# Performance work log

Measured on AMD Instinct MI355X. Metric: run time of the kernel, lower is better.

Reference implementation:

```python
import jax, jax.numpy as jnp
import numpy as np

B, KL, XL, DIM, H, PB = 4, 128, 4096, 256, 8, 8
HD = DIM // H
SCALE = HD ** -0.5
N_DIS = 64 + 2


def setup_inputs() -> dict:
    key = jax.random.key(0)
    ks = jax.random.split(key, 10)
    x = jax.random.normal(ks[0], (B, XL, DIM), jnp.float32)
    kernal = jax.random.normal(ks[1], (B, KL, DIM), jnp.float32)
    rd = jax.random.randint(ks[2], (B, KL, XL), 0, N_DIS)
    polar_pos = jax.random.randint(ks[3], (B, KL, XL), 0, PB)
    att_mask = jax.random.uniform(ks[4], (B, H, XL, KL)) < 0.1
    W_qkv = jax.random.normal(ks[5], (DIM, 3 * DIM), jnp.float32) * 0.02
    dis_embed = jax.random.normal(ks[6], (N_DIS, H), jnp.float32) * 0.02
    polar_emb = jax.random.normal(ks[7], (PB, 1), jnp.float32) * 0.02
    W_proj = jax.random.normal(ks[8], (DIM, DIM), jnp.float32) * 0.02
    b_proj = jnp.zeros((DIM,), jnp.float32)
    return dict(x=x, kernal=kernal, rd=rd, polar_pos=polar_pos, att_mask=att_mask,
                W_qkv=W_qkv, dis_embed=dis_embed, polar_emb=polar_emb,
                W_proj=W_proj, b_proj=b_proj)


def _heads(t, h):
    b, n, d = t.shape
    return t.reshape(b, n, h, d // h).transpose(0, 2, 1, 3)  # b h n hd


def reference(x, kernal, rd, polar_pos, att_mask, W_qkv, dis_embed, polar_emb, W_proj, b_proj):
    b, xl, dim = x.shape
    kl = kernal.shape[1]
    h = H
    scale = (dim // h) ** -0.5

    q, k, v = [_heads(t, h) for t in jnp.split(x @ W_qkv, 3, axis=-1)]        # b h xl hd
    k_q, k_k, k_v = [_heads(t, h) for t in jnp.split(kernal @ W_qkv, 3, axis=-1)]  # b h kl hd

    rd_e = dis_embed[rd].transpose(0, 3, 1, 2)  # (b,kl,xl,h) -> (b,h,kl,xl)

    # kernel -> x attention scores
    k_x_attn = jnp.einsum('bhkd,bhxd->bhkx', k_q, k) * scale  # b h kl xl

    # main orientation: one-hot-weighted |attn| reduced over x, argmax over polar bins
    pp = jnp.broadcast_to(polar_pos[:, None], (b, h, kl, xl))  # b h kl xl
    polar_hot = jax.nn.one_hot(pp, PB, dtype=k_x_attn.dtype)   # b h kl xl o
    ori_sum = jnp.einsum('bhkx,bhkxo->bhko', jnp.abs(k_x_attn), polar_hot)
    main_ori = jnp.argmax(ori_sum, axis=-1)                    # b h kl
    new_polar = pp - main_ori[..., None]
    new_polar = jnp.where(new_polar < 0, new_polar + PB, new_polar)
    polar_bias = polar_emb[new_polar, 0]                       # b h kl xl

    mask_k = att_mask.transpose(0, 1, 3, 2)                    # b h kl xl
    k_x_attn = jnp.where(mask_k, jnp.asarray(-1e6, k_x_attn.dtype), k_x_attn)
    attn_k = jax.nn.softmax(k_x_attn + rd_e + polar_bias, axis=-1)
    k_out = jnp.einsum('bhkx,bhxd->bhkd', attn_k, v)
    k_out = k_out.transpose(0, 2, 1, 3).reshape(b, kl, dim) @ W_proj + b_proj

    # x -> kernel attention scores
    x_k_attn = jnp.einsum('bhxd,bhkd->bhxk', q, k_k) * scale   # b h xl kl
    x_k_attn = jnp.where(att_mask, jnp.asarray(-1e9, x_k_attn.dtype), x_k_attn)
    x_k_attn = jax.nn.softmax(x_k_attn + rd_e.transpose(0, 1, 3, 2)
                              + polar_bias.transpose(0, 1, 3, 2), axis=-1)
    x_out = jnp.einsum('bhxk,bhkd->bhxd', x_k_attn, k_v)
    x_out = x_out.transpose(0, 2, 1, 3).reshape(b, xl, dim) @ W_proj + b_proj

    return (x_out, k_out)
```

## Files before the change

kernel.cpp:

```cpp
#include <hip/hip_runtime.h>
#include <hip/hip_bf16.h>

#define B_    4
#define KL_   128
#define XL_   4096
#define DIM_  256
#define H_    8
#define HD_   32
#define PB_   8
#define NDIS_ 66
#define TDIM_ 768
#define SCALE_ 0.17677669529663687f
#define NS_   4
#define XCH_  (XL_ / NS_)
#define NCH_  64
#define KC2_  16

typedef float v4f __attribute__((ext_vector_type(4)));
typedef short v8s __attribute__((ext_vector_type(8)));

__device__ __forceinline__ unsigned short f2bf(float f) {
    __hip_bfloat16 h = __float2bfloat16(f);
    return __builtin_bit_cast(unsigned short, h);
}
__device__ __forceinline__ float bf2f(unsigned short u) {
    return __bfloat162float(__builtin_bit_cast(__hip_bfloat16, u));
}
__device__ __forceinline__ void cvt_hilo(float v, unsigned short& hi, unsigned short& lo) {
    hi = f2bf(v);
    lo = f2bf(v - bf2f(hi));
}

__global__ __launch_bounds__(256) void cvt_mat(const float* __restrict__ A,
                                               unsigned short* __restrict__ Ah,
                                               unsigned short* __restrict__ Al,
                                               size_t n4) {
    size_t i = ((size_t)blockIdx.x * 256 + threadIdx.x);
    if (i >= n4) return;
    float4 v = *(const float4*)&A[i * 4];
    ushort4 h, l;
    cvt_hilo(v.x, h.x, l.x);
    cvt_hilo(v.y, h.y, l.y);
    cvt_hilo(v.z, h.z, l.z);
    cvt_hilo(v.w, h.w, l.w);
    *(ushort4*)&Ah[i * 4] = h;
    *(ushort4*)&Al[i * 4] = l;
}

__global__ __launch_bounds__(256) void cvt_wT(const float* __restrict__ W,
                                              unsigned short* __restrict__ Wh,
                                              unsigned short* __restrict__ Wl,
                                              int K, int N) {
    int n = blockIdx.x, k = threadIdx.x;
    float v = W[(size_t)k * N + n];
    unsigned short h, l;
    cvt_hilo(v, h, l);
    Wh[(size_t)n * K + k] = h;
    Wl[(size_t)n * K + k] = l;
}

__global__ __launch_bounds__(256) void cvt_kq(const float* __restrict__ qkv_k,
                                              unsigned short* __restrict__ Kqh_g,
                                              unsigned short* __restrict__ Kql_g) {
    const int bh = blockIdx.x;
    const int b = bh >> 3, h = bh & 7;
    const int tid = threadIdx.x;
    const int k = tid >> 1, dg = (tid & 1) * 16;
    const float* src = &qkv_k[((size_t)(b * KL_ + k)) * TDIM_ + h * HD_ + dg];
    unsigned short hi[16], lo[16];
#pragma unroll
    for (int j4 = 0; j4 < 4; ++j4) {
        float4 v = *(const float4*)&src[j4 * 4];
        cvt_hilo(v.x, hi[j4 * 4 + 0], lo[j4 * 4 + 0]);
        cvt_hilo(v.y, hi[j4 * 4 + 1], lo[j4 * 4 + 1]);
        cvt_hilo(v.z, hi[j4 * 4 + 2], lo[j4 * 4 + 2]);
        cvt_hilo(v.w, hi[j4 * 4 + 3], lo[j4 * 4 + 3]);
    }
    unsigned short* dh = &Kqh_g[((size_t)bh * KL_ + k) * HD_ + dg];
    unsigned short* dl = &Kql_g[((size_t)bh * KL_ + k) * HD_ + dg];
    *(uint4*)&dh[0] = *(uint4*)&hi[0];
    *(uint4*)&dh[8] = *(uint4*)&hi[8];
    *(uint4*)&dl[0] = *(uint4*)&lo[0];
    *(uint4*)&dl[8] = *(uint4*)&lo[8];
}

__global__ __launch_bounds__(256) void gemm_mfma(const unsigned short* __restrict__ Ah,
                                                 const unsigned short* __restrict__ Al,
                                                 const unsigned short* __restrict__ Bh,
                                                 const unsigned short* __restrict__ Bl,
                                                 float* __restrict__ C,
                                                 const float* __restrict__ bias,
                                                 int M, int N, int K) {
    __shared__ __align__(16) unsigned short Ah_s[128][40];
    __shared__ __align__(16) unsigned short Al_s[128][40];
    __shared__ __align__(16) unsigned short Bh_s[128][40];
    __shared__ __align__(16) unsigned short Bl_s[128][40];
    const int tid = threadIdx.x;
    const int w = tid >> 6, lane = tid & 63;
    const int c = lane & 15, q = lane >> 4;
    const int bm = blockIdx.y * 128, bn = blockIdx.x * 128;
    const int srow = tid >> 1, shf = (tid & 1) * 16;

    v4f acc[2][8] = {};
    for (int k0 = 0; k0 < K; k0 += 32) {
        __syncthreads();
        {
            const size_t ab = (size_t)(bm + srow) * K + k0 + shf;
            *(uint4*)&Ah_s[srow][shf] = *(const uint4*)&Ah[ab];
            *(uint4*)&Ah_s[srow][shf + 8] = *(const uint4*)&Ah[ab + 8];
            *(uint4*)&Al_s[srow][shf] = *(const uint4*)&Al[ab];
            *(uint4*)&Al_s[srow][shf + 8] = *(const uint4*)&Al[ab + 8];
            const size_t bb = (size_t)(bn + srow) * K + k0 + shf;
            *(uint4*)&Bh_s[srow][shf] = *(const uint4*)&Bh[bb];
            *(uint4*)&Bh_s[srow][shf + 8] = *(const uint4*)&Bh[bb + 8];
            *(uint4*)&Bl_s[srow][shf] = *(const uint4*)&Bl[bb];
            *(uint4*)&Bl_s[srow][shf + 8] = *(const uint4*)&Bl[bb + 8];
        }
        __syncthreads();
        v8s afh[2], afl[2];
#pragma unroll
        for (int mt = 0; mt < 2; ++mt) {
            afh[mt] = *(v8s*)&Ah_s[w * 32 + mt * 16 + c][q * 8];
            afl[mt] = *(v8s*)&Al_s[w * 32 + mt * 16 + c][q * 8];
        }
#pragma unroll
        for (int nt = 0; nt < 8; ++nt) {
            v8s bfh = *(v8s*)&Bh_s[nt * 16 + c][q * 8];
            v8s bfl = *(v8s*)&Bl_s[nt * 16 + c][q * 8];
#pragma unroll
            for (int mt = 0; mt < 2; ++mt) {
                acc[mt][nt] = __builtin_amdgcn_mfma_f32_16x16x32_bf16(afl[mt], bfh, acc[mt][nt], 0, 0, 0);
                acc[mt][nt] = __builtin_amdgcn_mfma_f32_16x16x32_bf16(afh[mt], bfl, acc[mt][nt], 0, 0, 0);
                acc[mt][nt] = __builtin_amdgcn_mfma_f32_16x16x32_bf16(afh[mt], bfh, acc[mt][nt], 0, 0, 0);
            }
        }
    }
#pragma unroll
    for (int mt = 0; mt < 2; ++mt) {
#pragma unroll
        for (int nt = 0; nt < 8; ++nt) {
            int col = bn + nt * 16 + c;
            float bv = bias ? bias[col] : 0.0f;
#pragma unroll
            for (int r = 0; r < 4; ++r) {
                int row = bm + w * 32 + mt * 16 + q * 4 + r;
                C[(size_t)row * N + col] = acc[mt][nt][r] + bv;
            }
        }
    }
}

__global__ __launch_bounds__(256) void gemm64(const float* __restrict__ A,
                                              const float* __restrict__ Bw,
                                              float* __restrict__ C,
                                              const float* __restrict__ bias,
                                              int M, int N, int K) {
    __shared__ __align__(16) float As[16][68];
    __shared__ __align__(16) float Bs[16][64];
    const int tid = threadIdx.x;
    const int tx = tid & 15, ty = tid >> 4;
    const int bn = blockIdx.x * 64, bm = blockIdx.y * 64;
    const int am = tid >> 2, ac = tid & 3;
    float acc[4][4] = {};
    for (int k0 = 0; k0 < K; k0 += 16) {
        float4 a4 = *(const float4*)&A[(size_t)(bm + am) * K + k0 + ac * 4];
        As[ac * 4 + 0][am] = a4.x;
        As[ac * 4 + 1][am] = a4.y;
        As[ac * 4 + 2][am] = a4.z;
        As[ac * 4 + 3][am] = a4.w;
        *(float4*)&Bs[ty][tx * 4] = *(const float4*)&Bw[(size_t)(k0 + ty) * N + bn + tx * 4];
        __syncthreads();
#pragma unroll
        for (int kk = 0; kk < 16; ++kk) {
            float4 av = *(const float4*)&As[kk][ty * 4];
            float4 bv = *(const float4*)&Bs[kk][tx * 4];
            float a[4] = {av.x, av.y, av.z, av.w};
            float b[4] = {bv.x, bv.y, bv.z, bv.w};
#pragma unroll
            for (int i = 0; i < 4; ++i)
#pragma unroll
                for (int j = 0; j < 4; ++j) acc[i][j] += a[i] * b[j];
        }
        __syncthreads();
    }
#pragma unroll
    for (int i = 0; i < 4; ++i) {
        int m = bm + ty * 4 + i;
#pragma unroll
        for (int j = 0; j < 4; ++j) {
            int n = bn + tx * 4 + j;
            float v = acc[i][j];
            if (bias) v += bias[n];
            C[(size_t)m * N + n] = v;
        }
    }
}

__global__ __launch_bounds__(256) void score_bins_mfma3(const float* __restrict__ qkv_x,
                                                        const unsigned short* __restrict__ Kqh_g,
                                                        const unsigned short* __restrict__ Kql_g,
                                                        const int* __restrict__ rd,
                                                        const int* __restrict__ polar_pos,
                                                        const int* __restrict__ att_mask,
                                                        const float* __restrict__ dis_embed,
                                                        __hip_bfloat16* __restrict__ Sg,
                                                        float* __restrict__ binspart) {
    const int b = blockIdx.z, h = blockIdx.y, xc = blockIdx.x;
    const int x0 = xc * 64;
    const int tid = threadIdx.x;
    const int w = tid >> 6, lane = tid & 63;
    const int c15 = lane & 15, q = lane >> 4;
    const size_t bh = (size_t)(b * H_ + h);

    __shared__ unsigned int mskb[64][5];
    __shared__ float de_h[NDIS_];
    __shared__ float binsL[8][4][16][PB_];

    {
        int xr = tid >> 2, kg = tid & 3;
        size_t gb = (bh * XL_ + x0 + xr) * KL_ + kg * 32;
        unsigned bits = 0;
#pragma unroll
        for (int i = 0; i < 8; ++i) {
            int4 m4 = *(const int4*)&att_mask[gb + i * 4];
            bits |= (m4.x ? 1u : 0u) << (i * 4 + 0);
            bits |= (m4.y ? 1u : 0u) << (i * 4 + 1);
            bits |= (m4.z ? 1u : 0u) << (i * 4 + 2);
            bits |= (m4.w ? 1u : 0u) << (i * 4 + 3);
        }
        mskb[xr][kg] = bits;
    }
    if (tid < NDIS_) de_h[tid] = dis_embed[tid * H_ + h];
    __syncthreads();

    v8s axh, axl;
    {
        const float* src = &qkv_x[((size_t)b * XL_ + x0 + w * 16 + c15) * TDIM_ + DIM_ + h * HD_ + q * 8];
        float4 v0 = *(const float4*)&src[0];
        float4 v1 = *(const float4*)&src[4];
        float vv[8] = {v0.x, v0.y, v0.z, v0.w, v1.x, v1.y, v1.z, v1.w};
#pragma unroll
        for (int j = 0; j < 8; ++j) {
            unsigned short hi, lo;
            cvt_hilo(vv[j], hi, lo);
            ((short*)&axh)[j] = (short)hi;
            ((short*)&axl)[j] = (short)lo;
        }
    }

    const int xw = x0 + w * 16;

#pragma unroll
    for (int nt = 0; nt < 8; ++nt) {
        const int k = nt * 16 + c15;
        const size_t kqoff = (bh * KL_ + k) * HD_ + q * 8;
        v8s bqh = *(const v8s*)&Kqh_g[kqoff];
        v8s bql = *(const v8s*)&Kql_g[kqoff];
        v4f D = {0.f, 0.f, 0.f, 0.f};
        D = __builtin_amdgcn_mfma_f32_16x16x32_bf16(axl, bqh, D, 0, 0, 0);
        D = __builtin_amdgcn_mfma_f32_16x16x32_bf16(axh, bql, D, 0, 0, 0);
        D = __builtin_amdgcn_mfma_f32_16x16x32_bf16(axh, bqh, D, 0, 0, 0);

        const size_t rowoff = ((size_t)(b * KL_ + k)) * XL_ + xw + q * 4;
        int4 r4 = *(const int4*)&rd[rowoff];
        int4 p4 = *(const int4*)&polar_pos[rowoff];
        int rv[4] = {r4.x, r4.y, r4.z, r4.w};
        int pv[4] = {p4.x, p4.y, p4.z, p4.w};

        float bins[PB_] = {};
        ushort4 pack;
#pragma unroll
        for (int r = 0; r < 4; ++r) {
            float s = D[r] * SCALE_;
            float a = fabsf(s);
            int pp = pv[r];
#pragma unroll
            for (int pb = 0; pb < PB_; ++pb) bins[pb] += (pp == pb) ? a : 0.0f;
            int xloc = w * 16 + q * 4 + r;
            int mbit = (mskb[xloc][k >> 5] >> (k & 31)) & 1;
            float sp = (mbit ? -1e6f : s) + de_h[rv[r]];
            ((unsigned short*)&pack)[r] = f2bf(sp);
        }
        *(ushort4*)((unsigned short*)Sg + (bh * KL_ + k) * XL_ + xw + q * 4) = pack;

#pragma unroll
        for (int pb = 0; pb < PB_; ++pb) {
            bins[pb] += __shfl_xor(bins[pb], 16);
            bins[pb] += __shfl_xor(bins[pb], 32);
        }
        if (q == 0) {
#pragma unroll
            for (int pb = 0; pb < PB_; ++pb) binsL[nt][w][c15][pb] = bins[pb];
        }
    }
    __syncthreads();
    {
        int k = tid >> 1, half = tid & 1;
        int nt = k >> 4, c = k & 15;
        float4 s = {0.f, 0.f, 0.f, 0.f};
#pragma unroll
        for (int w4 = 0; w4 < 4; ++w4) {
            float4 v = *(float4*)&binsL[nt][w4][c][half * 4];
            s.x += v.x; s.y += v.y; s.z += v.z; s.w += v.w;
        }
        *(float4*)&binspart[(bh * KL_ + k) * (NCH_ * PB_) + xc * PB_ + half * 4] = s;
    }
}

__global__ __launch_bounds__(256) void bins_argmax(const float* __restrict__ binspart,
                                                   int* __restrict__ main_ori) {
    const int w = threadIdx.x >> 6, lane = threadIdx.x & 63;
    const int row = blockIdx.x * 4 + w;
    const float* bp = &binspart[(size_t)row * (NCH_ * PB_) + lane * PB_];
    float s[PB_];
#pragma unroll
    for (int pb = 0; pb < PB_; ++pb) s[pb] = bp[pb];
#pragma unroll
    for (int m = 1; m < 64; m <<= 1)
#pragma unroll
        for (int pb = 0; pb < PB_; ++pb) s[pb] += __shfl_xor(s[pb], m);
    if (lane == 0) {
        float best = s[0];
        int bi = 0;
#pragma unroll
        for (int pb = 1; pb < PB_; ++pb)
            if (s[pb] > best) { best = s[pb]; bi = pb; }
        main_ori[row] = bi;
    }
}

__global__ __launch_bounds__(256) void flash_cached2(const float* __restrict__ qkv_x,
                                                     const __hip_bfloat16* __restrict__ Sg,
                                                     const int* __restrict__ polar_pos,
                                                     const float* __restrict__ polar_emb,
                                                     const int* __restrict__ main_ori,
                                                     float* __restrict__ part) {
    const int b = blockIdx.z, h = blockIdx.y;
    const int kch = blockIdx.x / NS_, xc = blockIdx.x % NS_;
    const int k0 = kch * KC2_;
    const int tid = threadIdx.x;
    const int ki = tid >> 4, xt = tid & 15;

    __shared__ __align__(16) float4 vs[64][9];
    __shared__ int pol_s[KC2_][68];
    __shared__ float pe[PB_];

    if (tid < PB_) pe[tid] = polar_emb[tid];
    const size_t xbase = (size_t)b * XL_;
    const size_t bh = (size_t)(b * H_ + h);
    const size_t row_k = bh * KL_ + k0 + ki;
    const int mo = main_ori[row_k];
    const int xbeg = xc * XCH_;

    float l = 0.f;
    float4 acc[8] = {};
    __syncthreads();
    for (int t = 0; t < XCH_ / 64; ++t) {
        const int x0 = xbeg + t * 64;
        __syncthreads();
#pragma unroll
        for (int i = 0; i < 2; ++i) {
            int id = tid + 256 * i;
            int row = id >> 3, c = id & 7;
            vs[row][c] = *(const float4*)&qkv_x[(xbase + x0 + row) * TDIM_ + 2 * DIM_ + h * HD_ + c * 4];
        }
        {
            int kk = tid >> 4, c = tid & 15;
            *(int4*)&pol_s[kk][c * 4] =
                *(const int4*)&polar_pos[(size_t)(b * KL_ + k0 + kk) * XL_ + x0 + c * 4];
        }
        __syncthreads();
#pragma unroll
        for (int j = 0; j < 4; ++j) {
            int xl = xt + 16 * j;
            int x = x0 + xl;
            float sp = __bfloat162float(Sg[row_k * XL_ + x]);
            int pp = pol_s[ki][xl];
            int np = pp - mo;
            np += (np >> 31) & PB_;
            float p = __expf(sp + pe[np]);
            l += p;
#pragma unroll
            for (int c = 0; c < 8; ++c) {
                float4 v = vs[xl][c];
                acc[c].x += p * v.x; acc[c].y += p * v.y;
                acc[c].z += p * v.z; acc[c].w += p * v.w;
            }
        }
    }
#pragma unroll
    for (int m = 1; m < 16; m <<= 1) {
        l += __shfl_xor(l, m, 16);
#pragma unroll
        for (int c = 0; c < 8; ++c) {
            acc[c].x += __shfl_xor(acc[c].x, m, 16);
            acc[c].y += __shfl_xor(acc[c].y, m, 16);
            acc[c].z += __shfl_xor(acc[c].z, m, 16);
            acc[c].w += __shfl_xor(acc[c].w, m, 16);
        }
    }
    if (xt == 0) {
        float* dst = &part[(size_t)(row_k * NS_ + xc) * 36];
#pragma unroll
        for (int c = 0; c < 8; ++c) *(float4*)&dst[c * 4] = acc[c];
        dst[32] = l;
    }
}

__global__ __launch_bounds__(256) void merge_cached(const float* __restrict__ part,
                                                    float* __restrict__ kout_pre) {
    const int tid = threadIdx.x;
    const int ri = tid >> 5, d = tid & 31;
    const int row = blockIdx.x * 8 + ri;
    float l = 0.f, a = 0.f;
#pragma unroll
    for (int c = 0; c < NS_; ++c) {
        const float* p = &part[(size_t)(row * NS_ + c) * 36];
        l += p[32];
        a += p[d];
    }
    int k = row & (KL_ - 1);
    int bh = row >> 7;
    int h = bh & (H_ - 1), b = bh >> 3;
    kout_pre[(size_t)(b * KL_ + k) * DIM_ + h * HD_ + d] = a / l;
}

__global__ __launch_bounds__(256) void attn_x_mfma(const float* __restrict__ qkv_x,
                                                   const float* __restrict__ qkv_k,
                                                   const int* __restrict__ rd,
                                                   const int* __restrict__ polar_pos,
                                                   const int* __restrict__ att_mask,
                                                   const float* __restrict__ dis_embed,
                                                   const float* __restrict__ polar_emb,
                                                   const int* __restrict__ main_ori,
                                                   unsigned short* __restrict__ oh,
                                                   unsigned short* __restrict__ ol) {
    const int b = blockIdx.z, h = blockIdx.y;
    const int x0 = blockIdx.x * 64;
    const int tid = threadIdx.x;
    const int wave = tid >> 6, lane = tid & 63;
    const int c = lane & 15, q = lane >> 4;

    __shared__ __align__(16) unsigned short Kk_s[KL_][40];
    __shared__ __align__(16) unsigned short VT_s[HD_][136];
    __shared__ __align__(16) unsigned short P_s[4][16][136];
    __shared__ unsigned short rp_s[KL_][72];
    __shared__ float de_h[NDIS_];
    __shared__ float pe[PB_];
    __shared__ int mo_s[KL_];

    const size_t bh = (size_t)(b * H_ + h);
    if (tid < NDIS_) de_h[tid] = dis_embed[tid * H_ + h];
    if (tid < PB_) pe[tid] = polar_emb[tid];
    if (tid < KL_) mo_s[tid] = main_ori[bh * KL_ + tid];

    {
        int row = tid >> 1, half = tid & 1;
        const float* src = &qkv_k[(size_t)(b * KL_ + row) * TDIM_ + h * HD_ + half * 16];
#pragma unroll
        for (int j = 0; j < 16; ++j) Kk_s[row][half * 16 + j] = f2bf(src[DIM_ + j]);
#pragma unroll
        for (int j = 0; j < 16; ++j) VT_s[half * 16 + j][row] = f2bf(src[2 * DIM_ + j]);
    }
    __syncthreads();

#pragma unroll
    for (int i = 0; i < 8; ++i) {
        int id = tid + 256 * i;
        int k = id >> 4, cc = id & 15;
        size_t gb = (size_t)(b * KL_ + k) * XL_ + x0 + cc * 4;
        int4 r4 = *(const int4*)&rd[gb];
        int4 p4 = *(const int4*)&polar_pos[gb];
        int mo = mo_s[k];
        int n0 = p4.x - mo; n0 += (n0 >> 31) & PB_;
        int n1 = p4.y - mo; n1 += (n1 >> 31) & PB_;
        int n2 = p4.z - mo; n2 += (n2 >> 31) & PB_;
        int n3 = p4.w - mo; n3 += (n3 >> 31) & PB_;
        rp_s[k][cc * 4 + 0] = (unsigned short)(r4.x | (n0 << 8));
        rp_s[k][cc * 4 + 1] = (unsigned short)(r4.y | (n1 << 8));
        rp_s[k][cc * 4 + 2] = (unsigned short)(r4.z | (n2 << 8));
        rp_s[k][cc * 4 + 3] = (unsigned short)(r4.w | (n3 << 8));
    }
    __syncthreads();
#pragma unroll
    for (int i = 0; i < 8; ++i) {
        int id = tid + 256 * i;
        int xr = id >> 5, kc = id & 31;
        int4 m4 = *(const int4*)&att_mask[(bh * XL_ + x0 + xr) * KL_ + kc * 4];
        if (m4.x) rp_s[kc * 4 + 0][xr] |= 0x8000;
        if (m4.y) rp_s[kc * 4 + 1][xr] |= 0x8000;
        if (m4.z) rp_s[kc * 4 + 2][xr] |= 0x8000;
        if (m4.w) rp_s[kc * 4 + 3][xr] |= 0x8000;
    }
    __syncthreads();

    v8s aq;
    {
        const float* qp = &qkv_x[(size_t)(b * XL_ + x0 + wave * 16 + c) * TDIM_ + h * HD_ + q * 8];
        float4 q0 = *(const float4*)&qp[0];
        float4 q1 = *(const float4*)&qp[4];
        aq[0] = (short)f2bf(q0.x); aq[1] = (short)f2bf(q0.y);
        aq[2] = (short)f2bf(q0.z); aq[3] = (short)f2bf(q0.w);
        aq[4] = (short)f2bf(q1.x); aq[5] = (short)f2bf(q1.y);
        aq[6] = (short)f2bf(q1.z); aq[7] = (short)f2bf(q1.w);
    }

    v4f S[8];
#pragma unroll
    for (int t = 0; t < 8; ++t) {
        v8s bk = *(v8s*)&Kk_s[t * 16 + c][q * 8];
        S[t] = __builtin_amdgcn_mfma_f32_16x16x32_bf16(aq, bk, (v4f){0.f, 0.f, 0.f, 0.f}, 0, 0, 0);
    }

    const int xloc = wave * 16;
    float lr[4] = {0.f, 0.f, 0.f, 0.f};
#pragma unroll
    for (int t = 0; t < 8; ++t) {
#pragma unroll
        for (int r = 0; r < 4; ++r) {
            int krow = t * 16 + c;
            int xrow = q * 4 + r;
            unsigned short rp = rp_s[krow][xloc + xrow];
            float sval = S[t][r] * SCALE_;
            float tval = ((rp & 0x8000) ? -25.0f : sval) + de_h[rp & 0x7f] + pe[(rp >> 8) & 7];
            float p = __expf(tval);
            unsigned short pb = f2bf(p);
            P_s[wave][xrow][krow] = pb;
            lr[r] += bf2f(pb);
        }
    }
#pragma unroll
    for (int r = 0; r < 4; ++r) {
#pragma unroll
        for (int m = 1; m < 16; m <<= 1) lr[r] += __shfl_xor(lr[r], m);
    }
    __syncthreads();

    v4f O0 = {0.f, 0.f, 0.f, 0.f}, O1 = {0.f, 0.f, 0.f, 0.f};
#pragma unroll
    for (int kc = 0; kc < 4; ++kc) {
        v8s ap = *(v8s*)&P_s[wave][c][kc * 32 + q * 8];
        v8s bv0 = *(v8s*)&VT_s[c][kc * 32 + q * 8];
        v8s bv1 = *(v8s*)&VT_s[16 + c][kc * 32 + q * 8];
        O0 = __builtin_amdgcn_mfma_f32_16x16x32_bf16(ap, bv0, O0, 0, 0, 0);
        O1 = __builtin_amdgcn_mfma_f32_16x16x32_bf16(ap, bv1, O1, 0, 0, 0);
    }

#pragma unroll
    for (int r = 0; r < 4; ++r) {
        int xg = x0 + wave * 16 + q * 4 + r;
        float inv = 1.0f / lr[r];
        size_t obase = (size_t)(b * XL_ + xg) * DIM_ + h * HD_;
        float v0 = O0[r] * inv;
        float v1 = O1[r] * inv;
        unsigned short h0, l0, h1, l1;
        cvt_hilo(v0, h0, l0);
        cvt_hilo(v1, h1, l1);
        oh[obase + c] = h0;
        ol[obase + c] = l0;
        oh[obase + 16 + c] = h1;
        ol[obase + 16 + c] = l1;
    }
}

extern "C" void kernel_launch(void* const* d_in, const int* in_sizes, int n_in,
                              void* d_out, int out_size, void* d_ws, size_t ws_size,
                              hipStream_t stream) {
    const float* x         = (const float*)d_in[0];
    const float* kernal    = (const float*)d_in[1];
    const int* rd          = (const int*)d_in[2];
    const int* polar_pos   = (const int*)d_in[3];
    const int* att_mask    = (const int*)d_in[4];
    const float* W_qkv     = (const float*)d_in[5];
    const float* dis_embed = (const float*)d_in[6];
    const float* polar_emb = (const float*)d_in[7];
    const float* W_proj    = (const float*)d_in[8];
    const float* b_proj    = (const float*)d_in[9];
    float* out             = (float*)d_out;

    char* base = (char*)d_ws;
    size_t off = 0;
    auto alloc = [&](size_t bytes) { void* p = base + off; off = (off + bytes + 255) & ~255ULL; return p; };
    float* qkv_x    = (float*)alloc((size_t)B_ * XL_ * TDIM_ * 4);
    float* qkv_k    = (float*)alloc((size_t)B_ * KL_ * TDIM_ * 4);
    float* xout_pre = (float*)alloc((size_t)B_ * XL_ * DIM_ * 4);
    float* kout_pre = (float*)alloc((size_t)B_ * KL_ * DIM_ * 4);
    int* main_ori   = (int*)alloc(B_ * H_ * KL_ * 4);
    float* part     = (float*)alloc((size_t)B_ * H_ * KL_ * NS_ * 36 * 4);
    __hip_bfloat16* Sg = (__hip_bfloat16*)alloc((size_t)B_ * H_ * KL_ * XL_ * 2);
    unsigned short* wph = (unsigned short*)alloc((size_t)DIM_ * DIM_ * 2);
    unsigned short* wpl = (unsigned short*)alloc((size_t)DIM_ * DIM_ * 2);

    float* binspart = xout_pre;
    const size_t MX = (size_t)B_ * XL_;
    unsigned short* xh = (unsigned short*)Sg;
    unsigned short* xl_ = xh + MX * DIM_;
    unsigned short* wqh = (unsigned short*)part;
    unsigned short* wql = wqh + (size_t)TDIM_ * DIM_;
    unsigned short* kqh_g = wqh + 2 * (size_t)TDIM_ * DIM_;
    unsigned short* kql_g = kqh_g + (size_t)B_ * H_ * KL_ * HD_;
    unsigned short* oh = (unsigned short*)Sg;
    unsigned short* ol = oh + MX * DIM_;

    cvt_mat<<<dim3((MX * DIM_ / 4 + 255) / 256), 256, 0, stream>>>(x, xh, xl_, MX * DIM_ / 4);
    cvt_wT<<<dim3(TDIM_), DIM_, 0, stream>>>(W_qkv, wqh, wql, DIM_, TDIM_);
    cvt_wT<<<dim3(DIM_), DIM_, 0, stream>>>(W_proj, wph, wpl, DIM_, DIM_);

    gemm_mfma<<<dim3(TDIM_ / 128, MX / 128), 256, 0, stream>>>(
        xh, xl_, wqh, wql, qkv_x, nullptr, MX, TDIM_, DIM_);
    gemm64<<<dim3(TDIM_ / 64, (B_ * KL_) / 64), 256, 0, stream>>>(
        kernal, W_qkv, qkv_k, nullptr, B_ * KL_, TDIM_, DIM_);
    cvt_kq<<<dim3(B_ * H_), 256, 0, stream>>>(qkv_k, kqh_g, kql_g);

    score_bins_mfma3<<<dim3(NCH_, H_, B_), 256, 0, stream>>>(
        qkv_x, kqh_g, kql_g, rd, polar_pos, att_mask, dis_embed, Sg, binspart);
    bins_argmax<<<dim3(B_ * H_ * KL_ / 4), 256, 0, stream>>>(binspart, main_ori);
    flash_cached2<<<dim3((KL_ / KC2_) * NS_, H_, B_), 256, 0, stream>>>(
        qkv_x, Sg, polar_pos, polar_emb, main_ori, part);
    merge_cached<<<dim3(B_ * H_ * KL_ / 8), 256, 0, stream>>>(part, kout_pre);

    attn_x_mfma<<<dim3(XL_ / 64, H_, B_), 256, 0, stream>>>(
        qkv_x, qkv_k, rd, polar_pos, att_mask, dis_embed, polar_emb, main_ori, oh, ol);

    gemm_mfma<<<dim3(DIM_ / 128, MX / 128), 256, 0, stream>>>(
        oh, ol, wph, wpl, out, b_proj, MX, DIM_, DIM_);
    gemm64<<<dim3(DIM_ / 64, (B_ * KL_) / 64), 256, 0, stream>>>(
        kout_pre, W_proj, out + (size_t)B_ * XL_ * DIM_, b_proj, B_ * KL_, DIM_, DIM_);
}
```

Before: 362.7 us.

## Double x-tile per block in score kernel and prefetch next k-tile operands

The score/bins kernel now covers 128 x positions per block instead of 64, halving the grid and reusing each loaded Kq hi/lo fragment across two MFMA tiles. It also software-pipelines the k-tile loop by loading the next tile's Kq, rd and polar_pos values while computing the current one. The bins partial buffer shrinks to 32 chunks, so the argmax kernel reads only half its lanes. The cost is more registers per thread and fewer blocks, which may lower occupancy and latency hiding.

```diff
diff --git a/kernel.cpp b/kernel.cpp
--- a/kernel.cpp
+++ b/kernel.cpp
@@ -13,7 +13,7 @@
 #define SCALE_ 0.17677669529663687f
 #define NS_   4
 #define XCH_  (XL_ / NS_)
-#define NCH_  64
+#define NCH2_ 32
 #define KC2_  16
 
 typedef float v4f __attribute__((ext_vector_type(4)));
@@ -196,7 +196,7 @@
     }
 }
 
-__global__ __launch_bounds__(256) void score_bins_mfma3(const float* __restrict__ qkv_x,
+__global__ __launch_bounds__(256) void score_bins_mfma4(const float* __restrict__ qkv_x,
                                                         const unsigned short* __restrict__ Kqh_g,
                                                         const unsigned short* __restrict__ Kql_g,
                                                         const int* __restrict__ rd,
@@ -206,18 +206,20 @@
                                                         __hip_bfloat16* __restrict__ Sg,
                                                         float* __restrict__ binspart) {
     const int b = blockIdx.z, h = blockIdx.y, xc = blockIdx.x;
-    const int x0 = xc * 64;
+    const int x0 = xc * 128;
     const int tid = threadIdx.x;
     const int w = tid >> 6, lane = tid & 63;
     const int c15 = lane & 15, q = lane >> 4;
     const size_t bh = (size_t)(b * H_ + h);
 
-    __shared__ unsigned int mskb[64][5];
+    __shared__ unsigned int mskb[128][5];
     __shared__ float de_h[NDIS_];
     __shared__ float binsL[8][4][16][PB_];
 
-    {
-        int xr = tid >> 2, kg = tid & 3;
+#pragma unroll
+    for (int it = 0; it < 2; ++it) {
+        int id = tid + 256 * it;
+        int xr = id >> 2, kg = id & 3;
         size_t gb = (bh * XL_ + x0 + xr) * KL_ + kg * 32;
         unsigned bits = 0;
 #pragma unroll
@@ -233,9 +235,10 @@
     if (tid < NDIS_) de_h[tid] = dis_embed[tid * H_ + h];
     __syncthreads();
 
-    v8s axh, axl;
-    {
-        const float* src = &qkv_x[((size_t)b * XL_ + x0 + w * 16 + c15) * TDIM_ + DIM_ + h * HD_ + q * 8];
+    v8s axh[2], axl[2];
+#pragma unroll
+    for (int t = 0; t < 2; ++t) {
+        const float* src = &qkv_x[((size_t)b * XL_ + x0 + t * 64 + w * 16 + c15) * TDIM_ + DIM_ + h * HD_ + q * 8];
         float4 v0 = *(const float4*)&src[0];
         float4 v1 = *(const float4*)&src[4];
         float vv[8] = {v0.x, v0.y, v0.z, v0.w, v1.x, v1.y, v1.z, v1.w};
@@ -243,45 +246,61 @@
         for (int j = 0; j < 8; ++j) {
             unsigned short hi, lo;
             cvt_hilo(vv[j], hi, lo);
-            ((short*)&axh)[j] = (short)hi;
-            ((short*)&axl)[j] = (short)lo;
-        }
-    }
-
-    const int xw = x0 + w * 16;
-
-#pragma unroll
-    for (int nt = 0; nt < 8; ++nt) {
+            ((short*)&axh[t])[j] = (short)hi;
+            ((short*)&axl[t])[j] = (short)lo;
+        }
+    }
+
+    v8s bqh[2], bql[2];
+    int4 r4[2][2], p4[2][2];
+    auto load_nt = [&](int nt, int s) {
         const int k = nt * 16 + c15;
         const size_t kqoff = (bh * KL_ + k) * HD_ + q * 8;
-        v8s bqh = *(const v8s*)&Kqh_g[kqoff];
-        v8s bql = *(const v8s*)&Kql_g[kqoff];
-        v4f D = {0.f, 0.f, 0.f, 0.f};
-        D = __builtin_amdgcn_mfma_f32_16x16x32_bf16(axl, bqh, D, 0, 0, 0);
-        D = __builtin_amdgcn_mfma_f32_16x16x32_bf16(axh, bql, D, 0, 0, 0);
-        D = __builtin_amdgcn_mfma_f32_16x16x32_bf16(axh, bqh, D, 0, 0, 0);
-
-        const size_t rowoff = ((size_t)(b * KL_ + k)) * XL_ + xw + q * 4;
-        int4 r4 = *(const int4*)&rd[rowoff];
-        int4 p4 = *(const int4*)&polar_pos[rowoff];
-        int rv[4] = {r4.x, r4.y, r4.z, r4.w};
-        int pv[4] = {p4.x, p4.y, p4.z, p4.w};
+        bqh[s] = *(const v8s*)&Kqh_g[kqoff];
+        bql[s] = *(const v8s*)&Kql_g[kqoff];
+#pragma unroll
+        for (int t = 0; t < 2; ++t) {
+            const size_t rowoff = ((size_t)(b * KL_ + k)) * XL_ + x0 + t * 64 + w * 16 + q * 4;
+            r4[s][t] = *(const int4*)&rd[rowoff];
+            p4[s][t] = *(const int4*)&polar_pos[rowoff];
+        }
+    };
+    load_nt(0, 0);
+
+#pragma unroll
+    for (int nt = 0; nt < 8; ++nt) {
+        const int s = nt & 1;
+        if (nt < 7) load_nt(nt + 1, s ^ 1);
+
+        const int k = nt * 16 + c15;
+        v4f D[2] = {{0.f, 0.f, 0.f, 0.f}, {0.f, 0.f, 0.f, 0.f}};
+#pragma unroll
+        for (int t = 0; t < 2; ++t) {
+            D[t] = __builtin_amdgcn_mfma_f32_16x16x32_bf16(axl[t], bqh[s], D[t], 0, 0, 0);
+            D[t] = __builtin_amdgcn_mfma_f32_16x16x32_bf16(axh[t], bql[s], D[t], 0, 0, 0);
+            D[t] = __builtin_amdgcn_mfma_f32_16x16x32_bf16(axh[t], bqh[s], D[t], 0, 0, 0);
+        }
 
         float bins[PB_] = {};
-        ushort4 pack;
-#pragma unroll
-        for (int r = 0; r < 4; ++r) {
-            float s = D[r] * SCALE_;
-            float a = fabsf(s);
-            int pp = pv[r];
-#pragma unroll
-            for (int pb = 0; pb < PB_; ++pb) bins[pb] += (pp == pb) ? a : 0.0f;
-            int xloc = w * 16 + q * 4 + r;
-            int mbit = (mskb[xloc][k >> 5] >> (k & 31)) & 1;
-            float sp = (mbit ? -1e6f : s) + de_h[rv[r]];
-            ((unsigned short*)&pack)[r] = f2bf(sp);
-        }
-        *(ushort4*)((unsigned short*)Sg + (bh * KL_ + k) * XL_ + xw + q * 4) = pack;
+#pragma unroll
+        for (int t = 0; t < 2; ++t) {
+            int rv[4] = {r4[s][t].x, r4[s][t].y, r4[s][t].z, r4[s][t].w};
+            int pv[4] = {p4[s][t].x, p4[s][t].y, p4[s][t].z, p4[s][t].w};
+            ushort4 pack;
+#pragma unroll
+            for (int r = 0; r < 4; ++r) {
+                float sc = D[t][r] * SCALE_;
+                float a = fabsf(sc);
+                int pp = pv[r];
+#pragma unroll
+                for (int pb = 0; pb < PB_; ++pb) bins[pb] += (pp == pb) ? a : 0.0f;
+                int xloc = t * 64 + w * 16 + q * 4 + r;
+                int mbit = (mskb[xloc][k >> 5] >> (k & 31)) & 1;
+                float sp = (mbit ? -1e6f : sc) + de_h[rv[r]];
+                ((unsigned short*)&pack)[r] = f2bf(sp);
+            }
+            *(ushort4*)((unsigned short*)Sg + (bh * KL_ + k) * XL_ + x0 + t * 64 + w * 16 + q * 4) = pack;
+        }
 
 #pragma unroll
         for (int pb = 0; pb < PB_; ++pb) {
@@ -303,7 +322,7 @@
             float4 v = *(float4*)&binsL[nt][w4][c][half * 4];
             s.x += v.x; s.y += v.y; s.z += v.z; s.w += v.w;
         }
-        *(float4*)&binspart[(bh * KL_ + k) * (NCH_ * PB_) + xc * PB_ + half * 4] = s;
+        *(float4*)&binspart[(bh * KL_ + k) * (NCH2_ * PB_) + xc * PB_ + half * 4] = s;
     }
 }
 
@@ -311,10 +330,14 @@
                                                    int* __restrict__ main_ori) {
     const int w = threadIdx.x >> 6, lane = threadIdx.x & 63;
     const int row = blockIdx.x * 4 + w;
-    const float* bp = &binspart[(size_t)row * (NCH_ * PB_) + lane * PB_];
     float s[PB_];
 #pragma unroll
-    for (int pb = 0; pb < PB_; ++pb) s[pb] = bp[pb];
+    for (int pb = 0; pb < PB_; ++pb) s[pb] = 0.0f;
+    if (lane < NCH2_) {
+        const float* bp = &binspart[(size_t)row * (NCH2_ * PB_) + lane * PB_];
+#pragma unroll
+        for (int pb = 0; pb < PB_; ++pb) s[pb] = bp[pb];
+    }
 #pragma unroll
     for (int m = 1; m < 64; m <<= 1)
 #pragma unroll
@@ -612,7 +635,7 @@
         kernal, W_qkv, qkv_k, nullptr, B_ * KL_, TDIM_, DIM_);
     cvt_kq<<<dim3(B_ * H_), 256, 0, stream>>>(qkv_k, kqh_g, kql_g);
 
-    score_bins_mfma3<<<dim3(NCH_, H_, B_), 256, 0, stream>>>(
+    score_bins_mfma4<<<dim3(NCH2_, H_, B_), 256, 0, stream>>>(
         qkv_x, kqh_g, kql_g, rd, polar_pos, att_mask, dis_embed, Sg, binspart);
     bins_argmax<<<dim3(B_ * H_ * KL_ / 4), 256, 0, stream>>>(binspart, main_ori);
     flash_cached2<<<dim3((KL_ / KC2_) * NS_, H_, B_), 256, 0, stream>>>(
```

Measured after the change: 357.2 us. Within noise of the previous version (-1.5%).

## Software-pipeline global loads in score and flash kernels via register double buffering

Applied to the files above, without the earlier changes.

In the score/bins kernel, the next k-tile's Kq operands, rd and polar_pos vectors are now loaded into a second register set while the current tile's MFMAs and epilogue run. In the flash kernel, the next V and polar_pos tile is prefetched into registers after the current one is written to shared memory, so global latency overlaps the compute loop. This costs extra registers, which may reduce occupancy.

```diff
diff --git a/kernel.cpp b/kernel.cpp
--- a/kernel.cpp
+++ b/kernel.cpp
@@ -196,7 +196,7 @@
     }
 }
 
-__global__ __launch_bounds__(256) void score_bins_mfma3(const float* __restrict__ qkv_x,
+__global__ __launch_bounds__(256) void score_bins_mfma5(const float* __restrict__ qkv_x,
                                                         const unsigned short* __restrict__ Kqh_g,
                                                         const unsigned short* __restrict__ Kql_g,
                                                         const int* __restrict__ rd,
@@ -250,35 +250,45 @@
 
     const int xw = x0 + w * 16;
 
-#pragma unroll
-    for (int nt = 0; nt < 8; ++nt) {
+    v8s bqh[2], bql[2];
+    int4 r4[2], p4[2];
+    auto load_nt = [&](int nt, int s) {
         const int k = nt * 16 + c15;
         const size_t kqoff = (bh * KL_ + k) * HD_ + q * 8;
-        v8s bqh = *(const v8s*)&Kqh_g[kqoff];
-        v8s bql = *(const v8s*)&Kql_g[kqoff];
+        bqh[s] = *(const v8s*)&Kqh_g[kqoff];
+        bql[s] = *(const v8s*)&Kql_g[kqoff];
+        const size_t rowoff = ((size_t)(b * KL_ + k)) * XL_ + xw + q * 4;
+        r4[s] = *(const int4*)&rd[rowoff];
+        p4[s] = *(const int4*)&polar_pos[rowoff];
+    };
+    load_nt(0, 0);
+
+#pragma unroll
+    for (int nt = 0; nt < 8; ++nt) {
+        const int s = nt & 1;
+        if (nt < 7) load_nt(nt + 1, s ^ 1);
+
+        const int k = nt * 16 + c15;
         v4f D = {0.f, 0.f, 0.f, 0.f};
-        D = __builtin_amdgcn_mfma_f32_16x16x32_bf16(axl, bqh, D, 0, 0, 0);
-        D = __builtin_amdgcn_mfma_f32_16x16x32_bf16(axh, bql, D, 0, 0, 0);
-        D = __builtin_amdgcn_mfma_f32_16x16x32_bf16(axh, bqh, D, 0, 0, 0);
-
-        const size_t rowoff = ((size_t)(b * KL_ + k)) * XL_ + xw + q * 4;
-        int4 r4 = *(const int4*)&rd[rowoff];
-        int4 p4 = *(const int4*)&polar_pos[rowoff];
-        int rv[4] = {r4.x, r4.y, r4.z, r4.w};
-        int pv[4] = {p4.x, p4.y, p4.z, p4.w};
+        D = __builtin_amdgcn_mfma_f32_16x16x32_bf16(axl, bqh[s], D, 0, 0, 0);
+        D = __builtin_amdgcn_mfma_f32_16x16x32_bf16(axh, bql[s], D, 0, 0, 0);
+        D = __builtin_amdgcn_mfma_f32_16x16x32_bf16(axh, bqh[s], D, 0, 0, 0);
+
+        int rv[4] = {r4[s].x, r4[s].y, r4[s].z, r4[s].w};
+        int pv[4] = {p4[s].x, p4[s].y, p4[s].z, p4[s].w};
 
         float bins[PB_] = {};
         ushort4 pack;
 #pragma unroll
         for (int r = 0; r < 4; ++r) {
-            float s = D[r] * SCALE_;
-            float a = fabsf(s);
+            float sc = D[r] * SCALE_;
+            float a = fabsf(sc);
             int pp = pv[r];
 #pragma unroll
             for (int pb = 0; pb < PB_; ++pb) bins[pb] += (pp == pb) ? a : 0.0f;
             int xloc = w * 16 + q * 4 + r;
             int mbit = (mskb[xloc][k >> 5] >> (k & 31)) & 1;
-            float sp = (mbit ? -1e6f : s) + de_h[rv[r]];
+            float sp = (mbit ? -1e6f : sc) + de_h[rv[r]];
             ((unsigned short*)&pack)[r] = f2bf(sp);
         }
         *(ushort4*)((unsigned short*)Sg + (bh * KL_ + k) * XL_ + xw + q * 4) = pack;
@@ -329,7 +339,7 @@
     }
 }
 
-__global__ __launch_bounds__(256) void flash_cached2(const float* __restrict__ qkv_x,
+__global__ __launch_bounds__(256) void flash_cached3(const float* __restrict__ qkv_x,
                                                      const __hip_bfloat16* __restrict__ Sg,
                                                      const int* __restrict__ polar_pos,
                                                      const float* __restrict__ polar_emb,
@@ -352,23 +362,29 @@
     const int mo = main_ori[row_k];
     const int xbeg = xc * XCH_;
 
+    const int vrow0 = tid >> 3, vc0 = tid & 7;
+    const int vrow1 = 32 + (tid >> 3), vc1 = tid & 7;
+    const int pkk = tid >> 4, pcc = tid & 15;
+
+    float4 rv0, rv1;
+    int4 rp;
+    auto load_tile = [&](int t) {
+        const int x0 = xbeg + t * 64;
+        rv0 = *(const float4*)&qkv_x[(xbase + x0 + vrow0) * TDIM_ + 2 * DIM_ + h * HD_ + vc0 * 4];
+        rv1 = *(const float4*)&qkv_x[(xbase + x0 + vrow1) * TDIM_ + 2 * DIM_ + h * HD_ + vc1 * 4];
+        rp = *(const int4*)&polar_pos[(size_t)(b * KL_ + k0 + pkk) * XL_ + x0 + pcc * 4];
+    };
+    load_tile(0);
+
     float l = 0.f;
     float4 acc[8] = {};
-    __syncthreads();
     for (int t = 0; t < XCH_ / 64; ++t) {
         const int x0 = xbeg + t * 64;
         __syncthreads();
-#pragma unroll
-        for (int i = 0; i < 2; ++i) {
-            int id = tid + 256 * i;
-            int row = id >> 3, c = id & 7;
-            vs[row][c] = *(const float4*)&qkv_x[(xbase + x0 + row) * TDIM_ + 2 * DIM_ + h * HD_ + c * 4];
-        }
-        {
-            int kk = tid >> 4, c = tid & 15;
-            *(int4*)&pol_s[kk][c * 4] =
-                *(const int4*)&polar_pos[(size_t)(b * KL_ + k0 + kk) * XL_ + x0 + c * 4];
-        }
+        vs[vrow0][vc0] = rv0;
+        vs[vrow1][vc1] = rv1;
+        *(int4*)&pol_s[pkk][pcc * 4] = rp;
+        if (t + 1 < XCH_ / 64) load_tile(t + 1);
         __syncthreads();
 #pragma unroll
         for (int j = 0; j < 4; ++j) {
@@ -612,10 +628,10 @@
         kernal, W_qkv, qkv_k, nullptr, B_ * KL_, TDIM_, DIM_);
     cvt_kq<<<dim3(B_ * H_), 256, 0, stream>>>(qkv_k, kqh_g, kql_g);
 
-    score_bins_mfma3<<<dim3(NCH_, H_, B_), 256, 0, stream>>>(
+    score_bins_mfma5<<<dim3(NCH_, H_, B_), 256, 0, stream>>>(
         qkv_x, kqh_g, kql_g, rd, polar_pos, att_mask, dis_embed, Sg, binspart);
     bins_argmax<<<dim3(B_ * H_ * KL_ / 4), 256, 0, stream>>>(binspart, main_ori);
-    flash_cached2<<<dim3((KL_ / KC2_) * NS_, H_, B_), 256, 0, stream>>>(
+    flash_cached3<<<dim3((KL_ / KC2_) * NS_, H_, B_), 256, 0, stream>>>(
         qkv_x, Sg, polar_pos, polar_emb, main_ori, part);
     merge_cached<<<dim3(B_ * H_ * KL_ / 8), 256, 0, stream>>>(part, kout_pre);
 
```

New measurement: 362.3 us. Within noise of the previous version (-0.1%).
